# Kernel tuning notes

Measured on AMD Instinct MI355X. Metric: run time of the kernel, lower is better.

The kernel has to match this reference:

```python
import jax, jax.numpy as jnp
import numpy as np

N = 50000        # nodes
E = 1600000      # edges (avg degree 32)
F_IN = 512       # input features
HID = 8          # hidden per head (hardcoded in module)
HEADS = 8        # in_head (hardcoded in module)
CLS = 16         # num_classes
NEG_SLOPE = 0.2  # PyG GATConv default


def setup_inputs() -> dict:
    key = jax.random.key(0)
    ks = jax.random.split(key, 12)
    s = 0.05
    return {
        "x": jax.random.normal(ks[0], (N, F_IN), dtype=jnp.float32),
        "edge_index": jax.random.randint(ks[1], (2, E), 0, N, dtype=jnp.int64),
        "W1": jax.random.normal(ks[2], (F_IN, HEADS * HID), dtype=jnp.float32) * s,
        "att_src1": jax.random.normal(ks[3], (HEADS, HID), dtype=jnp.float32) * s,
        "att_dst1": jax.random.normal(ks[4], (HEADS, HID), dtype=jnp.float32) * s,
        "bias1": jax.random.normal(ks[5], (HEADS * HID,), dtype=jnp.float32) * s,
        "W2": jax.random.normal(ks[6], (HEADS * HID, CLS), dtype=jnp.float32) * s,
        "att_src2": jax.random.normal(ks[7], (1, CLS), dtype=jnp.float32) * s,
        "att_dst2": jax.random.normal(ks[8], (1, CLS), dtype=jnp.float32) * s,
        "bias2": jax.random.normal(ks[9], (CLS,), dtype=jnp.float32) * s,
    }


def _gat_conv(x, src, dst, W, att_src, att_dst, bias, n, heads, ch, concat):
    # Linear projection: [n, heads, ch]
    h = (x @ W).reshape(n, heads, ch)
    # Per-node attention logits (PyG style): alpha_src/dst = sum(h * a)
    a_src = jnp.einsum("nhc,hc->nh", h, att_src)  # [n, heads]
    a_dst = jnp.einsum("nhc,hc->nh", h, att_dst)
    # Per-edge raw score, leaky_relu, then segment softmax over incoming edges per dst
    e = jax.nn.leaky_relu(a_src[src] + a_dst[dst], NEG_SLOPE)  # [Etot, heads]
    m = jax.ops.segment_max(e, dst, num_segments=n)            # [n, heads]
    w = jnp.exp(e - m[dst])
    den = jax.ops.segment_sum(w, dst, num_segments=n)
    alpha = w / den[dst]                                        # [Etot, heads]
    # Scatter-aggregate weighted source features
    out = jax.ops.segment_sum(h[src] * alpha[..., None], dst, num_segments=n)  # [n, heads, ch]
    out = out.reshape(n, heads * ch) if concat else out.mean(axis=1)
    return out + bias


def reference(x, edge_index, W1, att_src1, att_dst1, bias1, W2, att_src2, att_dst2, bias2):
    n = x.shape[0]
    # PyG GATConv adds self-loops by default
    loops = jnp.arange(n, dtype=edge_index.dtype)
    src = jnp.concatenate([edge_index[0], loops])
    dst = jnp.concatenate([edge_index[1], loops])
    # dropout(p=0.6) is identity in eval mode
    h = _gat_conv(x, src, dst, W1, att_src1, att_dst1, bias1, n, HEADS, HID, True)
    h = jax.nn.elu(h)
    out = _gat_conv(h, src, dst, W2, att_src2, att_dst2, bias2, n, 1, CLS, False)
    return jax.nn.log_softmax(out, axis=1)
```

## Files before the change

kernel.cpp:

```cpp
#include <hip/hip_runtime.h>
#include <cstddef>

#define N_NODES 50000
#define N_EDGES 1600000
#define N_ETOT  (N_EDGES + N_NODES)
#define F_IN    512
#define HEADS   8
#define HID     8
#define CLS     16

#define NBUCK   196
#define BCAP    12288
#define CHUNKA  4096

typedef float v4 __attribute__((ext_vector_type(4)));
typedef float v2 __attribute__((ext_vector_type(2)));
typedef unsigned short us4 __attribute__((ext_vector_type(4)));
typedef unsigned int u4 __attribute__((ext_vector_type(4)));
typedef short bfrag __attribute__((ext_vector_type(8)));
typedef float ffrag __attribute__((ext_vector_type(4)));

__device__ inline float b2f_lo(unsigned int u) { return __uint_as_float(u << 16); }
__device__ inline float b2f_hi(unsigned int u) { return __uint_as_float(u & 0xffff0000u); }
__device__ inline v2 up2(unsigned int u) {
  v2 r;
  r[0] = __uint_as_float(u << 16);
  r[1] = __uint_as_float(u & 0xffff0000u);
  return r;
}
__device__ inline unsigned short f2b(float f) {
  unsigned int x = __float_as_uint(f);
  unsigned int r = (x + 0x7fffu + ((x >> 16) & 1u)) >> 16;
  return (unsigned short)r;
}

__global__ __launch_bounds__(256) void w1t_kernel(
    const float* __restrict__ W, unsigned short* __restrict__ WT,
    int* __restrict__ gcur) {
  int t = threadIdx.x;
  if (blockIdx.x == 128) {
    if (t < NBUCK) gcur[t] = 0;
    return;
  }
  int i = blockIdx.x * 256 + t;
  int k = i >> 6, n = i & 63;
  WT[n * F_IN + k] = f2b(W[i]);
}

__global__ __launch_bounds__(256) void gemm1_kernel(
    const float* __restrict__ x, const unsigned short* __restrict__ W1bT,
    const float* __restrict__ att_src, const float* __restrict__ att_dst,
    unsigned short* __restrict__ h1b, float* __restrict__ a_src,
    float* __restrict__ a_dst, int nrows) {
  __shared__ unsigned short xsb[64][72];
  __shared__ unsigned short wsb[64][72];
  int t = threadIdx.x;
  int lane = t & 63;
  int w = t >> 6;
  int row0 = blockIdx.x * 64;
  ffrag acc[4];
  acc[0] = 0.f; acc[1] = 0.f; acc[2] = 0.f; acc[3] = 0.f;

  int mrow = lane & 15;
  int koff = (lane >> 4) * 8;

  for (int kt = 0; kt < 8; ++kt) {
    int k0 = kt * 64;
#pragma unroll
    for (int r = 0; r < 4; ++r) {
      int slot = t + r * 256;
      int m = slot >> 4;
      int k4 = (slot & 15) * 4;
      v4 v = 0.f;
      int grow = row0 + m;
      if (grow < nrows) v = *(const v4*)(x + (size_t)grow * F_IN + k0 + k4);
      us4 o;
      o.x = f2b(v[0]); o.y = f2b(v[1]); o.z = f2b(v[2]); o.w = f2b(v[3]);
      *(us4*)&xsb[m][k4] = o;
    }
#pragma unroll
    for (int r = 0; r < 2; ++r) {
      int slot = t + r * 256;
      int nn = slot >> 3;
      int k8 = (slot & 7) * 8;
      *(bfrag*)&wsb[nn][k8] = *(const bfrag*)(W1bT + nn * F_IN + k0 + k8);
    }
    __syncthreads();
#pragma unroll
    for (int kk = 0; kk < 64; kk += 32) {
      bfrag a = *(const bfrag*)&xsb[w * 16 + mrow][kk + koff];
#pragma unroll
      for (int tt = 0; tt < 4; ++tt) {
        bfrag b = *(const bfrag*)&wsb[tt * 16 + mrow][kk + koff];
        acc[tt] = __builtin_amdgcn_mfma_f32_16x16x32_bf16(a, b, acc[tt], 0, 0, 0);
      }
    }
    __syncthreads();
  }
  int c = lane & 15, q = lane >> 4;
  float as_[4], ad_[4];
#pragma unroll
  for (int tt = 0; tt < 4; ++tt) {
    as_[tt] = att_src[tt * 16 + c];
    ad_[tt] = att_dst[tt * 16 + c];
  }
#pragma unroll
  for (int r = 0; r < 4; ++r) {
    int grow = row0 + w * 16 + q * 4 + r;
    float ps[4], pd[4];
#pragma unroll
    for (int tt = 0; tt < 4; ++tt) {
      ps[tt] = acc[tt][r] * as_[tt];
      pd[tt] = acc[tt][r] * ad_[tt];
    }
#pragma unroll
    for (int o = 1; o < 8; o <<= 1) {
#pragma unroll
      for (int tt = 0; tt < 4; ++tt) {
        ps[tt] += __shfl_xor(ps[tt], o);
        pd[tt] += __shfl_xor(pd[tt], o);
      }
    }
    if (grow < nrows) {
#pragma unroll
      for (int tt = 0; tt < 4; ++tt)
        h1b[(size_t)grow * 64 + tt * 16 + c] = f2b(acc[tt][r]);
      if ((c & 7) == 0) {
#pragma unroll
        for (int tt = 0; tt < 4; ++tt) {
          int head = tt * 2 + (c >> 3);
          a_src[grow * 8 + head] = ps[tt];
          a_dst[grow * 8 + head] = pd[tt];
        }
      }
    }
  }
}

__global__ __launch_bounds__(256) void bucketA_kernel(
    const int* __restrict__ src_idx, const int* __restrict__ dst_idx,
    int* __restrict__ gcur, int* __restrict__ abuck) {
  __shared__ int hist[NBUCK];
  __shared__ int base[NBUCK];
  __shared__ int cur[NBUCK];
  int t = threadIdx.x;
  if (t < NBUCK) hist[t] = 0;
  __syncthreads();
  int e0 = blockIdx.x * CHUNKA;
  int eend = e0 + CHUNKA;
  if (eend > N_EDGES) eend = N_EDGES;
  for (int e = e0 + t; e < eend; e += 256)
    atomicAdd(&hist[(unsigned)dst_idx[e] >> 8], 1);
  __syncthreads();
  if (t < NBUCK) {
    int c = hist[t];
    base[t] = c ? atomicAdd(&gcur[t], c) : 0;
    cur[t] = 0;
  }
  __syncthreads();
  for (int e = e0 + t; e < eend; e += 256) {
    int s = src_idx[e];
    int d = dst_idx[e];
    int b = (unsigned)d >> 8;
    int r = atomicAdd(&cur[b], 1);
    abuck[b * BCAP + base[b] + r] = (s << 8) | (d & 255);
  }
}

__global__ __launch_bounds__(256) void bucketB_kernel(
    const int* __restrict__ gcur, const int* __restrict__ abuck,
    int* __restrict__ indptr, unsigned short* __restrict__ csr16) {
  __shared__ int gs[256];
  __shared__ int hist[256];
  __shared__ int sm[256];
  __shared__ int cur[256];
  int b = blockIdx.x;
  int t = threadIdx.x;
  int gv = (t < NBUCK) ? gcur[t] : 0;
  gs[t] = gv;
  __syncthreads();
  for (int o = 1; o < 256; o <<= 1) {
    int u = (t >= o) ? gs[t - o] : 0;
    __syncthreads();
    gs[t] += u;
    __syncthreads();
  }
  int bbase = (b > 0 ? gs[b - 1] : 0) + 256 * b;
  int M = gcur[b];
  int node0 = b * 256;
  int nnodes = N_NODES - node0;
  if (nnodes > 256) nnodes = 256;
  hist[t] = (t < nnodes) ? 1 : 0;
  __syncthreads();
  const int* ab = abuck + b * BCAP;
  for (int i = t; i < M; i += 256)
    atomicAdd(&hist[ab[i] & 255], 1);
  __syncthreads();
  int v = hist[t];
  sm[t] = v;
  __syncthreads();
  for (int o = 1; o < 256; o <<= 1) {
    int u = (t >= o) ? sm[t - o] : 0;
    __syncthreads();
    sm[t] += u;
    __syncthreads();
  }
  int excl = sm[t] - v;
  cur[t] = excl;
  if (t < nnodes) indptr[node0 + t] = bbase + excl;
  if (b == NBUCK - 1 && t == 0) indptr[N_NODES] = N_ETOT;
  __syncthreads();
  for (int i = t; i < M; i += 256) {
    int entry = ab[i];
    int r = atomicAdd(&cur[entry & 255], 1);
    csr16[bbase + r] = (unsigned short)((unsigned)entry >> 8);
  }
  if (t < nnodes) {
    int r = atomicAdd(&cur[t], 1);
    csr16[bbase + r] = (unsigned short)(node0 + t);
  }
}

__global__ __launch_bounds__(256) void agg1_kernel(
    const int* __restrict__ indptr, const unsigned short* __restrict__ csr16,
    const unsigned short* __restrict__ h1b, const float* __restrict__ a_src1,
    const float* __restrict__ a_dst1, const float* __restrict__ bias1,
    float* __restrict__ h_elu, int n) {
  int wave = threadIdx.x >> 6;
  int lane = threadIdx.x & 63;
  int node = blockIdx.x * 4 + wave;
  if (node >= n) return;
  int j = lane >> 3;
  int h = lane & 7;
  float adst = a_dst1[(unsigned)(node * 8 + h)];
  int beg = indptr[node], end = indptr[node + 1];
  v2 acc[4];
  acc[0] = 0.f; acc[1] = 0.f; acc[2] = 0.f; acc[3] = 0.f;
  float den = 0.f;
  for (int base = beg; base < end; base += 64) {
    int m = end - base;
    if (m > 64) m = 64;
    int sv = (lane < m) ? (int)csr16[base + lane] : 0;
    for (int p = 0; p < m; p += 16) {
      int ia = p + j, ib = p + 8 + j;
      int sa = __shfl(sv, ia & 63);
      int sb = __shfl(sv, ib & 63);
      bool aa = ia < m, ab = ib < m;
      float ga = a_src1[(unsigned)(sa * 8 + h)];
      float gb = a_src1[(unsigned)(sb * 8 + h)];
      u4 fa = *(const u4*)(h1b + (unsigned)(sa * 64 + h * 8));
      u4 fb = *(const u4*)(h1b + (unsigned)(sb * 64 + h * 8));
      float ea = ga + adst, eb = gb + adst;
      ea = fmaxf(ea, 0.2f * ea);
      eb = fmaxf(eb, 0.2f * eb);
      float wa = aa ? __expf(ea) : 0.f;
      float wb = ab ? __expf(eb) : 0.f;
      den += wa + wb;
      v2 wa2, wb2;
      wa2[0] = wa; wa2[1] = wa;
      wb2[0] = wb; wb2[1] = wb;
      acc[0] += wa2 * up2(fa.x); acc[1] += wa2 * up2(fa.y);
      acc[2] += wa2 * up2(fa.z); acc[3] += wa2 * up2(fa.w);
      acc[0] += wb2 * up2(fb.x); acc[1] += wb2 * up2(fb.y);
      acc[2] += wb2 * up2(fb.z); acc[3] += wb2 * up2(fb.w);
    }
  }
#pragma unroll
  for (int o = 8; o < 64; o <<= 1) {
    den += __shfl_xor(den, o);
#pragma unroll
    for (int i = 0; i < 4; ++i) {
      acc[i][0] += __shfl_xor(acc[i][0], o);
      acc[i][1] += __shfl_xor(acc[i][1], o);
    }
  }
  if (j == 0) {
    float inv = 1.f / den;
    v4 b0 = *(const v4*)(bias1 + h * 8);
    v4 b1 = *(const v4*)(bias1 + h * 8 + 4);
    v4 o0, o1;
    o0[0] = acc[0][0] * inv + b0[0]; o0[1] = acc[0][1] * inv + b0[1];
    o0[2] = acc[1][0] * inv + b0[2]; o0[3] = acc[1][1] * inv + b0[3];
    o1[0] = acc[2][0] * inv + b1[0]; o1[1] = acc[2][1] * inv + b1[1];
    o1[2] = acc[3][0] * inv + b1[2]; o1[3] = acc[3][1] * inv + b1[3];
#pragma unroll
    for (int k = 0; k < 4; ++k) {
      o0[k] = (o0[k] > 0.f) ? o0[k] : (__expf(o0[k]) - 1.f);
      o1[k] = (o1[k] > 0.f) ? o1[k] : (__expf(o1[k]) - 1.f);
    }
    *(v4*)(h_elu + (size_t)node * 64 + h * 8)     = o0;
    *(v4*)(h_elu + (size_t)node * 64 + h * 8 + 4) = o1;
  }
}

__global__ __launch_bounds__(256) void gemm2_kernel(
    const float* __restrict__ h_elu, const float* __restrict__ W2,
    const float* __restrict__ att_src2, const float* __restrict__ att_dst2,
    unsigned short* __restrict__ h2b, float* __restrict__ a_src2,
    float* __restrict__ a_dst2, int n) {
  __shared__ float xs[64][68];
  __shared__ float ws[64][16];
  int t = threadIdx.x;
  int row0 = blockIdx.x * 64;
  {
    int k = t >> 2, c4 = (t & 3) * 4;
    *(v4*)&ws[k][c4] = *(const v4*)(W2 + (size_t)k * 16 + c4);
  }
#pragma unroll
  for (int r = 0; r < 4; ++r) {
    int idx = t + r * 256;
    int m = idx >> 4;
    int c4 = (idx & 15) * 4;
    v4 v = 0.f;
    int grow = row0 + m;
    if (grow < n) v = *(const v4*)(h_elu + (size_t)grow * 64 + c4);
    *(v4*)&xs[m][c4] = v;
  }
  __syncthreads();
  int r = t >> 2, q = t & 3;
  int grow = row0 + r;
  v4 acc = 0.f;
#pragma unroll
  for (int k = 0; k < 64; ++k) {
    acc += xs[r][k] * *(const v4*)&ws[k][q * 4];
  }
  v4 asv = *(const v4*)(att_src2 + q * 4);
  v4 adv = *(const v4*)(att_dst2 + q * 4);
  float ps = acc[0] * asv[0] + acc[1] * asv[1] + acc[2] * asv[2] + acc[3] * asv[3];
  float pd = acc[0] * adv[0] + acc[1] * adv[1] + acc[2] * adv[2] + acc[3] * adv[3];
  ps += __shfl_xor(ps, 1); ps += __shfl_xor(ps, 2);
  pd += __shfl_xor(pd, 1); pd += __shfl_xor(pd, 2);
  if (grow < n) {
    us4 o;
    o.x = f2b(acc[0]); o.y = f2b(acc[1]); o.z = f2b(acc[2]); o.w = f2b(acc[3]);
    *(us4*)(h2b + (size_t)grow * 16 + q * 4) = o;
    if (q == 0) { a_src2[grow] = ps; a_dst2[grow] = pd; }
  }
}

__global__ __launch_bounds__(256) void agg2_kernel(
    const int* __restrict__ indptr, const unsigned short* __restrict__ csr16,
    const unsigned short* __restrict__ h2b, const float* __restrict__ a_src2,
    const float* __restrict__ a_dst2, const float* __restrict__ bias2,
    float* __restrict__ out, int n) {
  int wave = threadIdx.x >> 6;
  int lane = threadIdx.x & 63;
  int node = blockIdx.x * 4 + wave;
  if (node >= n) return;
  int j = lane >> 3;
  int sub = lane & 7;
  float adst = a_dst2[node];
  int beg = indptr[node], end = indptr[node + 1];
  float acc0 = 0.f, acc1 = 0.f, den = 0.f;
  for (int base = beg; base < end; base += 64) {
    int m = end - base;
    if (m > 64) m = 64;
    int sv = (lane < m) ? (int)csr16[base + lane] : 0;
    for (int p = 0; p < m; p += 16) {
      int ia = p + j, ib = p + 8 + j;
      int sa = __shfl(sv, ia & 63);
      int sb = __shfl(sv, ib & 63);
      bool aa = ia < m, ab = ib < m;
      float ga = a_src2[(unsigned)sa];
      float gb = a_src2[(unsigned)sb];
      unsigned fa = *(const unsigned*)(h2b + (unsigned)(sa * 16 + sub * 2));
      unsigned fb = *(const unsigned*)(h2b + (unsigned)(sb * 16 + sub * 2));
      float ea = ga + adst, eb = gb + adst;
      ea = fmaxf(ea, 0.2f * ea);
      eb = fmaxf(eb, 0.2f * eb);
      float wa = aa ? __expf(ea) : 0.f;
      float wb = ab ? __expf(eb) : 0.f;
      den += wa + wb;
      acc0 += wa * b2f_lo(fa) + wb * b2f_lo(fb);
      acc1 += wa * b2f_hi(fa) + wb * b2f_hi(fb);
    }
  }
#pragma unroll
  for (int o = 8; o < 64; o <<= 1) {
    den  += __shfl_xor(den, o);
    acc0 += __shfl_xor(acc0, o);
    acc1 += __shfl_xor(acc1, o);
  }
  float inv = 1.f / den;
  float v0 = acc0 * inv + bias2[sub * 2];
  float v1 = acc1 * inv + bias2[sub * 2 + 1];
  float mx = fmaxf(v0, v1);
#pragma unroll
  for (int o = 1; o < 8; o <<= 1) mx = fmaxf(mx, __shfl_xor(mx, o));
  float ss = __expf(v0 - mx) + __expf(v1 - mx);
#pragma unroll
  for (int o = 1; o < 8; o <<= 1) ss += __shfl_xor(ss, o);
  float lg = mx + __logf(ss);
  if (j == 0) {
    v2 r;
    r[0] = v0 - lg;
    r[1] = v1 - lg;
    *(v2*)(out + (size_t)node * 16 + sub * 2) = r;
  }
}

extern "C" void kernel_launch(void* const* d_in, const int* in_sizes, int n_in,
                              void* d_out, int out_size, void* d_ws, size_t ws_size,
                              hipStream_t stream) {
  const float* x        = (const float*)d_in[0];
  const int*   ei       = (const int*)d_in[1];
  const float* W1       = (const float*)d_in[2];
  const float* att_src1 = (const float*)d_in[3];
  const float* att_dst1 = (const float*)d_in[4];
  const float* bias1    = (const float*)d_in[5];
  const float* W2       = (const float*)d_in[6];
  const float* att_src2 = (const float*)d_in[7];
  const float* att_dst2 = (const float*)d_in[8];
  const float* bias2    = (const float*)d_in[9];
  const int* src_idx = ei;
  const int* dst_idx = ei + N_EDGES;

  char* p = (char*)d_ws;
  auto alloc = [&](size_t bytes) {
    void* r = (void*)p;
    p += (bytes + 255) & ~(size_t)255;
    return r;
  };
  unsigned short* h1b = (unsigned short*)alloc((size_t)N_NODES * 64 * 2);
  float* h_elu   = (float*)alloc((size_t)N_NODES * 64 * 4);
  float* a_src1  = (float*)alloc((size_t)N_NODES * 8 * 4);
  float* a_dst1  = (float*)alloc((size_t)N_NODES * 8 * 4);
  unsigned short* h2b = (unsigned short*)alloc((size_t)N_NODES * 16 * 2);
  float* a_src2  = (float*)alloc((size_t)N_NODES * 4);
  float* a_dst2  = (float*)alloc((size_t)N_NODES * 4);
  int* indptr    = (int*)alloc((size_t)(N_NODES + 1) * 4);
  int* gcur      = (int*)alloc((size_t)NBUCK * 4);
  unsigned short* csr16 = (unsigned short*)alloc((size_t)N_ETOT * 2);
  unsigned short* W1bT  = (unsigned short*)alloc((size_t)64 * F_IN * 2);
  int* abuck     = (int*)h_elu;

  w1t_kernel<<<129, 256, 0, stream>>>(W1, W1bT, gcur);
  gemm1_kernel<<<(N_NODES + 63) / 64, 256, 0, stream>>>(
      x, W1bT, att_src1, att_dst1, h1b, a_src1, a_dst1, N_NODES);

  bucketA_kernel<<<(N_EDGES + CHUNKA - 1) / CHUNKA, 256, 0, stream>>>(
      src_idx, dst_idx, gcur, abuck);
  bucketB_kernel<<<NBUCK, 256, 0, stream>>>(gcur, abuck, indptr, csr16);

  agg1_kernel<<<N_NODES / 4, 256, 0, stream>>>(
      indptr, csr16, h1b, a_src1, a_dst1, bias1, h_elu, N_NODES);

  gemm2_kernel<<<(N_NODES + 63) / 64, 256, 0, stream>>>(
      h_elu, W2, att_src2, att_dst2, h2b, a_src2, a_dst2, N_NODES);

  agg2_kernel<<<N_NODES / 4, 256, 0, stream>>>(
      indptr, csr16, h2b, a_src2, a_dst2, bias2, (float*)d_out, N_NODES);
}
```

Baseline: 296.8 us.

## Merge gemm1 and edge bucketing into one launch; unroll gather loops by four

Folds the bucketA edge-binning work into the gemm1 launch as extra blocks, so the compute-bound projection and the atomic-heavy bucketing run concurrently in a single grid instead of as two serial launches. It also unrolls the aggregation loops in agg1 and agg2 to process four neighbor groups per iteration, putting more independent gathers in flight. The merged kernel carries both sets of shared memory, which may lower occupancy, and the wider unroll raises register pressure.

New measurement: 282.7 us. -4.7%, faster.

```diff
diff --git a/kernel.cpp b/kernel.cpp
--- a/kernel.cpp
+++ b/kernel.cpp
@@ -12,6 +12,8 @@
 #define NBUCK   196
 #define BCAP    12288
 #define CHUNKA  4096
+#define NB_GEMM1 782
+#define NB_BUCKA 391
 
 typedef float v4 __attribute__((ext_vector_type(4)));
 typedef float v2 __attribute__((ext_vector_type(2)));
@@ -22,12 +24,6 @@
 
 __device__ inline float b2f_lo(unsigned int u) { return __uint_as_float(u << 16); }
 __device__ inline float b2f_hi(unsigned int u) { return __uint_as_float(u & 0xffff0000u); }
-__device__ inline v2 up2(unsigned int u) {
-  v2 r;
-  r[0] = __uint_as_float(u << 16);
-  r[1] = __uint_as_float(u & 0xffff0000u);
-  return r;
-}
 __device__ inline unsigned short f2b(float f) {
   unsigned int x = __float_as_uint(f);
   unsigned int r = (x + 0x7fffu + ((x >> 16) & 1u)) >> 16;
@@ -47,14 +43,46 @@
   WT[n * F_IN + k] = f2b(W[i]);
 }
 
-__global__ __launch_bounds__(256) void gemm1_kernel(
+__global__ __launch_bounds__(256) void gemm1_bucketA_kernel(
     const float* __restrict__ x, const unsigned short* __restrict__ W1bT,
     const float* __restrict__ att_src, const float* __restrict__ att_dst,
     unsigned short* __restrict__ h1b, float* __restrict__ a_src,
-    float* __restrict__ a_dst, int nrows) {
+    float* __restrict__ a_dst, int nrows,
+    const int* __restrict__ src_idx, const int* __restrict__ dst_idx,
+    int* __restrict__ gcur, int* __restrict__ abuck) {
   __shared__ unsigned short xsb[64][72];
   __shared__ unsigned short wsb[64][72];
+  __shared__ int hist[NBUCK];
+  __shared__ int base[NBUCK];
+  __shared__ int cur[NBUCK];
   int t = threadIdx.x;
+
+  if (blockIdx.x >= NB_GEMM1) {
+    if (t < NBUCK) hist[t] = 0;
+    __syncthreads();
+    int blk = blockIdx.x - NB_GEMM1;
+    int e0 = blk * CHUNKA;
+    int eend = e0 + CHUNKA;
+    if (eend > N_EDGES) eend = N_EDGES;
+    for (int e = e0 + t; e < eend; e += 256)
+      atomicAdd(&hist[(unsigned)dst_idx[e] >> 8], 1);
+    __syncthreads();
+    if (t < NBUCK) {
+      int c = hist[t];
+      base[t] = c ? atomicAdd(&gcur[t], c) : 0;
+      cur[t] = 0;
+    }
+    __syncthreads();
+    for (int e = e0 + t; e < eend; e += 256) {
+      int s = src_idx[e];
+      int d = dst_idx[e];
+      int b = (unsigned)d >> 8;
+      int r = atomicAdd(&cur[b], 1);
+      abuck[b * BCAP + base[b] + r] = (s << 8) | (d & 255);
+    }
+    return;
+  }
+
   int lane = t & 63;
   int w = t >> 6;
   int row0 = blockIdx.x * 64;
@@ -134,36 +162,6 @@
         }
       }
     }
-  }
-}
-
-__global__ __launch_bounds__(256) void bucketA_kernel(
-    const int* __restrict__ src_idx, const int* __restrict__ dst_idx,
-    int* __restrict__ gcur, int* __restrict__ abuck) {
-  __shared__ int hist[NBUCK];
-  __shared__ int base[NBUCK];
-  __shared__ int cur[NBUCK];
-  int t = threadIdx.x;
-  if (t < NBUCK) hist[t] = 0;
-  __syncthreads();
-  int e0 = blockIdx.x * CHUNKA;
-  int eend = e0 + CHUNKA;
-  if (eend > N_EDGES) eend = N_EDGES;
-  for (int e = e0 + t; e < eend; e += 256)
-    atomicAdd(&hist[(unsigned)dst_idx[e] >> 8], 1);
-  __syncthreads();
-  if (t < NBUCK) {
-    int c = hist[t];
-    base[t] = c ? atomicAdd(&gcur[t], c) : 0;
-    cur[t] = 0;
-  }
-  __syncthreads();
-  for (int e = e0 + t; e < eend; e += 256) {
-    int s = src_idx[e];
-    int d = dst_idx[e];
-    int b = (unsigned)d >> 8;
-    int r = atomicAdd(&cur[b], 1);
-    abuck[b * BCAP + base[b] + r] = (s << 8) | (d & 255);
   }
 }
 
@@ -241,28 +239,55 @@
     int m = end - base;
     if (m > 64) m = 64;
     int sv = (lane < m) ? (int)csr16[base + lane] : 0;
-    for (int p = 0; p < m; p += 16) {
-      int ia = p + j, ib = p + 8 + j;
-      int sa = __shfl(sv, ia & 63);
-      int sb = __shfl(sv, ib & 63);
-      bool aa = ia < m, ab = ib < m;
-      float ga = a_src1[(unsigned)(sa * 8 + h)];
-      float gb = a_src1[(unsigned)(sb * 8 + h)];
-      u4 fa = *(const u4*)(h1b + (unsigned)(sa * 64 + h * 8));
-      u4 fb = *(const u4*)(h1b + (unsigned)(sb * 64 + h * 8));
-      float ea = ga + adst, eb = gb + adst;
-      ea = fmaxf(ea, 0.2f * ea);
-      eb = fmaxf(eb, 0.2f * eb);
-      float wa = aa ? __expf(ea) : 0.f;
-      float wb = ab ? __expf(eb) : 0.f;
-      den += wa + wb;
-      v2 wa2, wb2;
-      wa2[0] = wa; wa2[1] = wa;
-      wb2[0] = wb; wb2[1] = wb;
-      acc[0] += wa2 * up2(fa.x); acc[1] += wa2 * up2(fa.y);
-      acc[2] += wa2 * up2(fa.z); acc[3] += wa2 * up2(fa.w);
-      acc[0] += wb2 * up2(fb.x); acc[1] += wb2 * up2(fb.y);
-      acc[2] += wb2 * up2(fb.z); acc[3] += wb2 * up2(fb.w);
+    for (int p = 0; p < m; p += 32) {
+      int i0 = p + j, i1 = p + 8 + j, i2 = p + 16 + j, i3 = p + 24 + j;
+      int s0 = __shfl(sv, i0);
+      int s1 = __shfl(sv, i1);
+      int s2 = __shfl(sv, i2);
+      int s3 = __shfl(sv, i3);
+      bool a0 = i0 < m, a1 = i1 < m, a2 = i2 < m, a3 = i3 < m;
+      float g0 = a_src1[(unsigned)(s0 * 8 + h)];
+      float g1 = a_src1[(unsigned)(s1 * 8 + h)];
+      float g2 = a_src1[(unsigned)(s2 * 8 + h)];
+      float g3 = a_src1[(unsigned)(s3 * 8 + h)];
+      u4 f0 = *(const u4*)(h1b + (unsigned)(s0 * 64 + h * 8));
+      u4 f1 = *(const u4*)(h1b + (unsigned)(s1 * 64 + h * 8));
+      u4 f2 = *(const u4*)(h1b + (unsigned)(s2 * 64 + h * 8));
+      u4 f3 = *(const u4*)(h1b + (unsigned)(s3 * 64 + h * 8));
+      float e0 = g0 + adst, e1 = g1 + adst, e2 = g2 + adst, e3 = g3 + adst;
+      e0 = fmaxf(e0, 0.2f * e0); e1 = fmaxf(e1, 0.2f * e1);
+      e2 = fmaxf(e2, 0.2f * e2); e3 = fmaxf(e3, 0.2f * e3);
+      float w0 = a0 ? __expf(e0) : 0.f;
+      float w1 = a1 ? __expf(e1) : 0.f;
+      float w2 = a2 ? __expf(e2) : 0.f;
+      float w3 = a3 ? __expf(e3) : 0.f;
+      den += (w0 + w1) + (w2 + w3);
+      v2 w0v, w1v, w2v, w3v;
+      w0v[0] = w0; w0v[1] = w0;
+      w1v[0] = w1; w1v[1] = w1;
+      w2v[0] = w2; w2v[1] = w2;
+      w3v[0] = w3; w3v[1] = w3;
+      v2 t0, t1, t2, t3;
+      t0[0] = b2f_lo(f0.x); t0[1] = b2f_hi(f0.x);
+      t1[0] = b2f_lo(f1.x); t1[1] = b2f_hi(f1.x);
+      t2[0] = b2f_lo(f2.x); t2[1] = b2f_hi(f2.x);
+      t3[0] = b2f_lo(f3.x); t3[1] = b2f_hi(f3.x);
+      acc[0] += w0v * t0 + w1v * t1 + w2v * t2 + w3v * t3;
+      t0[0] = b2f_lo(f0.y); t0[1] = b2f_hi(f0.y);
+      t1[0] = b2f_lo(f1.y); t1[1] = b2f_hi(f1.y);
+      t2[0] = b2f_lo(f2.y); t2[1] = b2f_hi(f2.y);
+      t3[0] = b2f_lo(f3.y); t3[1] = b2f_hi(f3.y);
+      acc[1] += w0v * t0 + w1v * t1 + w2v * t2 + w3v * t3;
+      t0[0] = b2f_lo(f0.z); t0[1] = b2f_hi(f0.z);
+      t1[0] = b2f_lo(f1.z); t1[1] = b2f_hi(f1.z);
+      t2[0] = b2f_lo(f2.z); t2[1] = b2f_hi(f2.z);
+      t3[0] = b2f_lo(f3.z); t3[1] = b2f_hi(f3.z);
+      acc[2] += w0v * t0 + w1v * t1 + w2v * t2 + w3v * t3;
+      t0[0] = b2f_lo(f0.w); t0[1] = b2f_hi(f0.w);
+      t1[0] = b2f_lo(f1.w); t1[1] = b2f_hi(f1.w);
+      t2[0] = b2f_lo(f2.w); t2[1] = b2f_hi(f2.w);
+      t3[0] = b2f_lo(f3.w); t3[1] = b2f_hi(f3.w);
+      acc[3] += w0v * t0 + w1v * t1 + w2v * t2 + w3v * t3;
     }
   }
 #pragma unroll
@@ -356,23 +381,31 @@
     int m = end - base;
     if (m > 64) m = 64;
     int sv = (lane < m) ? (int)csr16[base + lane] : 0;
-    for (int p = 0; p < m; p += 16) {
-      int ia = p + j, ib = p + 8 + j;
-      int sa = __shfl(sv, ia & 63);
-      int sb = __shfl(sv, ib & 63);
-      bool aa = ia < m, ab = ib < m;
-      float ga = a_src2[(unsigned)sa];
-      float gb = a_src2[(unsigned)sb];
-      unsigned fa = *(const unsigned*)(h2b + (unsigned)(sa * 16 + sub * 2));
-      unsigned fb = *(const unsigned*)(h2b + (unsigned)(sb * 16 + sub * 2));
-      float ea = ga + adst, eb = gb + adst;
-      ea = fmaxf(ea, 0.2f * ea);
-      eb = fmaxf(eb, 0.2f * eb);
-      float wa = aa ? __expf(ea) : 0.f;
-      float wb = ab ? __expf(eb) : 0.f;
-      den += wa + wb;
-      acc0 += wa * b2f_lo(fa) + wb * b2f_lo(fb);
-      acc1 += wa * b2f_hi(fa) + wb * b2f_hi(fb);
+    for (int p = 0; p < m; p += 32) {
+      int i0 = p + j, i1 = p + 8 + j, i2 = p + 16 + j, i3 = p + 24 + j;
+      int s0 = __shfl(sv, i0);
+      int s1 = __shfl(sv, i1);
+      int s2 = __shfl(sv, i2);
+      int s3 = __shfl(sv, i3);
+      bool a0 = i0 < m, a1 = i1 < m, a2 = i2 < m, a3 = i3 < m;
+      float g0 = a_src2[(unsigned)s0];
+      float g1 = a_src2[(unsigned)s1];
+      float g2 = a_src2[(unsigned)s2];
+      float g3 = a_src2[(unsigned)s3];
+      unsigned f0 = *(const unsigned*)(h2b + (unsigned)(s0 * 16 + sub * 2));
+      unsigned f1 = *(const unsigned*)(h2b + (unsigned)(s1 * 16 + sub * 2));
+      unsigned f2 = *(const unsigned*)(h2b + (unsigned)(s2 * 16 + sub * 2));
+      unsigned f3 = *(const unsigned*)(h2b + (unsigned)(s3 * 16 + sub * 2));
+      float e0 = g0 + adst, e1 = g1 + adst, e2 = g2 + adst, e3 = g3 + adst;
+      e0 = fmaxf(e0, 0.2f * e0); e1 = fmaxf(e1, 0.2f * e1);
+      e2 = fmaxf(e2, 0.2f * e2); e3 = fmaxf(e3, 0.2f * e3);
+      float w0 = a0 ? __expf(e0) : 0.f;
+      float w1 = a1 ? __expf(e1) : 0.f;
+      float w2 = a2 ? __expf(e2) : 0.f;
+      float w3 = a3 ? __expf(e3) : 0.f;
+      den += (w0 + w1) + (w2 + w3);
+      acc0 += w0 * b2f_lo(f0) + w1 * b2f_lo(f1) + w2 * b2f_lo(f2) + w3 * b2f_lo(f3);
+      acc1 += w0 * b2f_hi(f0) + w1 * b2f_hi(f1) + w2 * b2f_hi(f2) + w3 * b2f_hi(f3);
     }
   }
 #pragma unroll
@@ -435,11 +468,11 @@
   int* abuck     = (int*)h_elu;
 
   w1t_kernel<<<129, 256, 0, stream>>>(W1, W1bT, gcur);
-  gemm1_kernel<<<(N_NODES + 63) / 64, 256, 0, stream>>>(
-      x, W1bT, att_src1, att_dst1, h1b, a_src1, a_dst1, N_NODES);
-
-  bucketA_kernel<<<(N_EDGES + CHUNKA - 1) / CHUNKA, 256, 0, stream>>>(
+
+  gemm1_bucketA_kernel<<<NB_GEMM1 + NB_BUCKA, 256, 0, stream>>>(
+      x, W1bT, att_src1, att_dst1, h1b, a_src1, a_dst1, N_NODES,
       src_idx, dst_idx, gcur, abuck);
+
   bucketB_kernel<<<NBUCK, 256, 0, stream>>>(gcur, abuck, indptr, csr16);
 
   agg1_kernel<<<N_NODES / 4, 256, 0, stream>>>(
```
